# Kernel tuning notes

Hardware: AMD Instinct MI355X
Metric: run time of the kernel (lower is better)

Reference implementation:

```python
import jax, jax.numpy as jnp
import numpy as np
import math

B, D, C_LEN, Q_LEN = 32, 128, 1024, 256
NEG = -1e30

def setup_inputs() -> dict:
    key = jax.random.key(0)
    ks = jax.random.split(key, 8)
    bound = 1.0 / math.sqrt(D)
    return {
        "C": jax.random.normal(ks[0], (B, D, C_LEN), jnp.float32),
        "Q": jax.random.normal(ks[1], (B, D, Q_LEN), jnp.float32),
        "c_mask": jnp.ones((B, C_LEN), jnp.float32),
        "q_mask": jnp.ones((B, Q_LEN), jnp.float32),
        "W0": jax.random.uniform(ks[2], (3 * D,), jnp.float32, -bound, bound),
        # depthwise conv1d: in=4D groups=4D kernel=5 -> weight (4D, 1, 5)
        "dw_w": jax.random.normal(ks[3], (4 * D, 1, 5), jnp.float32) * math.sqrt(2.0 / 5),
        "dw_b": jnp.zeros((4 * D,), jnp.float32),
        # pointwise conv1d: 4D -> D, kernel 1
        "pw_w": jax.random.normal(ks[4], (D, 4 * D, 1), jnp.float32) * math.sqrt(2.0 / (4 * D)),
        "pw_b": jnp.zeros((D,), jnp.float32),
    }

def reference(C, Q, c_mask, q_mask, W0, dw_w, dw_b, pw_w, pw_b):
    d = W0.shape[0] // 3
    C_t = jnp.swapaxes(C, 1, 2)  # (B, c_len, d)
    Q_t = jnp.swapaxes(Q, 1, 2)  # (B, q_len, d)
    w1, w2, w3 = W0[:d], W0[d:2 * d], W0[2 * d:]
    # Trilinear similarity without materializing (B,c,q,3d):
    # S[b,i,j] = C_t[b,i].w1 + Q_t[b,j].w2 + sum_k C_t[b,i,k]*Q_t[b,j,k]*w3[k]
    S = (jnp.einsum('bik,bjk->bij', C_t * w3, Q_t)
         + (C_t @ w1)[:, :, None] + (Q_t @ w2)[:, None, :])  # (B, c_len, q_len)
    q_m = q_mask[:, None, :]
    c_m = c_mask[:, :, None]
    S_bar = jax.nn.softmax(S * q_m + NEG * (1.0 - q_m), axis=2)
    S_bbar = jax.nn.softmax(S * c_m + NEG * (1.0 - c_m), axis=1)
    A = jnp.einsum('bij,bjk->bik', S_bar, Q_t)                       # (B, c_len, d)
    # bmm(S_bar, S_bbar^T) @ C_t  ==  S_bar @ (S_bbar^T @ C_t)
    Bm = jnp.einsum('bij,bjk->bik', S_bar, jnp.einsum('bij,bik->bjk', S_bbar, C_t))
    out = jnp.concatenate([C_t, A, C_t * A, C_t * Bm], axis=2)       # (B, c_len, 4d)
    x = jnp.swapaxes(out, 1, 2)  # (B, 4d, c_len)
    # depthwise separable conv (eval mode: dropout is identity)
    x = jax.lax.conv_general_dilated(x, dw_w, (1,), [(2, 2)],
                                     dimension_numbers=('NCH', 'OIH', 'NCH'),
                                     feature_group_count=x.shape[1]) + dw_b[None, :, None]
    x = jax.lax.conv_general_dilated(x, pw_w, (1,), [(0, 0)],
                                     dimension_numbers=('NCH', 'OIH', 'NCH')) + pw_b[None, :, None]
    return x  # (B, d, c_len)
```

## Files before the change

### kernel.cpp

```cpp
#include <hip/hip_runtime.h>
#include <math.h>

#define NB 32
#define ND 128
#define NC 1024
#define NQ 256
#define NEGV (-1e30f)

typedef __attribute__((ext_vector_type(8))) __bf16 bf16x8;
typedef __attribute__((ext_vector_type(4))) float f32x4;
typedef __attribute__((ext_vector_type(8))) unsigned short u16x8;
typedef __attribute__((ext_vector_type(4))) unsigned short u16x4;

__device__ inline unsigned short f2bf(float f) {
  unsigned u = __builtin_bit_cast(unsigned, f);
  u += 0x7FFFu + ((u >> 16) & 1u);
  return (unsigned short)(u >> 16);
}
__device__ inline float bf2f(unsigned short u) {
  return __builtin_bit_cast(float, (unsigned)u << 16);
}

__global__ __launch_bounds__(256) void k_pwcvt(const float* __restrict__ pwW, unsigned short* __restrict__ pwB16) {
  int idx = blockIdx.x * 256 + threadIdx.x;
  const float4* src = (const float4*)pwW;
  float4 v0 = src[idx * 2], v1 = src[idx * 2 + 1];
  u16x8 o;
  o[0] = f2bf(v0.x); o[1] = f2bf(v0.y); o[2] = f2bf(v0.z); o[3] = f2bf(v0.w);
  o[4] = f2bf(v1.x); o[5] = f2bf(v1.y); o[6] = f2bf(v1.z); o[7] = f2bf(v1.w);
  ((u16x8*)pwB16)[idx] = o;
}

__global__ __launch_bounds__(256) void k_qprep(const float* __restrict__ Q, const float* __restrict__ W0,
                                               unsigned short* __restrict__ qSwz, unsigned short* __restrict__ qT,
                                               float* __restrict__ qb) {
  __shared__ unsigned short T2[128 * 66];
  __shared__ float w2L[128];
  __shared__ float qbP[4][64];
  int b = blockIdx.y, jc = blockIdx.x, j0 = jc * 64, t = threadIdx.x;
  if (t < 128) w2L[t] = W0[ND + t];
  int d = t >> 1, half = t & 1;
  const float* src = Q + ((size_t)b * ND + d) * NQ + j0 + half * 32;
  unsigned short* qdst = qSwz + ((size_t)b * ND + d) * NQ + jc * 64;
  #pragma unroll
  for (int q = 0; q < 4; ++q) {
    float4 v0 = ((const float4*)src)[q * 2];
    float4 v1 = ((const float4*)src)[q * 2 + 1];
    u16x8 o;
    o[0] = f2bf(v0.x); o[1] = f2bf(v0.y); o[2] = f2bf(v0.z); o[3] = f2bf(v0.w);
    o[4] = f2bf(v1.x); o[5] = f2bf(v1.y); o[6] = f2bf(v1.z); o[7] = f2bf(v1.w);
    *(u16x8*)&T2[d * 66 + half * 32 + q * 8] = o;
    int g = half * 4 + q;
    *(u16x8*)&qdst[(g ^ (d & 7)) * 8] = o;
  }
  __syncthreads();
  {
    int jj = t & 63, dq = t >> 6;
    float s = 0.f;
    #pragma unroll 8
    for (int k = 0; k < 32; ++k) {
      int dd = dq * 32 + k;
      s += bf2f(T2[dd * 66 + jj]) * w2L[dd];
    }
    qbP[dq][jj] = s;
  }
  __syncthreads();
  if (t < 64)
    qb[b * NQ + j0 + t] = qbP[0][t] + qbP[1][t] + qbP[2][t] + qbP[3][t];
  {
    int jj = t >> 2, p = t & 3;
    unsigned short* dst = qT + ((size_t)b * NQ + j0 + jj) * ND;
    #pragma unroll
    for (int q = 0; q < 4; ++q) {
      int g = p * 4 + q;
      u16x8 o;
      #pragma unroll
      for (int e = 0; e < 8; ++e) o[e] = T2[(g * 8 + e) * 66 + jj];
      int sg = (g & 8) | ((g & 7) ^ (jj & 7));
      *(u16x8*)&dst[sg * 8] = o;
    }
  }
}

__global__ __launch_bounds__(256) void k_cprep(const float* __restrict__ C, const float* __restrict__ W0,
                                               unsigned short* __restrict__ cw3T, unsigned short* __restrict__ cSwz,
                                               float* __restrict__ cb) {
  __shared__ unsigned short T2[128 * 66];
  __shared__ float w1L[128], w3L[128];
  __shared__ float cbP[4][64];
  int b = blockIdx.y, i0 = blockIdx.x * 64, t = threadIdx.x;
  if (t < 128) { w1L[t] = W0[t]; w3L[t] = W0[2 * ND + t]; }
  int k = t >> 1, half = t & 1;
  const float* src = C + ((size_t)b * ND + k) * NC + i0 + half * 32;
  unsigned short* cdst = cSwz + ((size_t)b * ND + k) * NC + blockIdx.x * 64;
  #pragma unroll
  for (int q = 0; q < 4; ++q) {
    float4 v0 = ((const float4*)src)[q * 2];
    float4 v1 = ((const float4*)src)[q * 2 + 1];
    u16x8 o;
    o[0] = f2bf(v0.x); o[1] = f2bf(v0.y); o[2] = f2bf(v0.z); o[3] = f2bf(v0.w);
    o[4] = f2bf(v1.x); o[5] = f2bf(v1.y); o[6] = f2bf(v1.z); o[7] = f2bf(v1.w);
    *(u16x8*)&T2[k * 66 + half * 32 + q * 8] = o;
    int g = half * 4 + q;
    *(u16x8*)&cdst[(g ^ (k & 7)) * 8] = o;
  }
  __syncthreads();
  {
    int ii = t & 63, kq = t >> 6;
    float s = 0.f;
    #pragma unroll 8
    for (int kk = 0; kk < 32; ++kk) {
      int dd = kq * 32 + kk;
      s += bf2f(T2[dd * 66 + ii]) * w1L[dd];
    }
    cbP[kq][ii] = s;
  }
  __syncthreads();
  if (t < 64)
    cb[b * NC + i0 + t] = cbP[0][t] + cbP[1][t] + cbP[2][t] + cbP[3][t];
  {
    int ii = t >> 2, p = t & 3;
    unsigned short* dst = cw3T + ((size_t)b * NC + i0 + ii) * ND;
    #pragma unroll
    for (int q = 0; q < 4; ++q) {
      int g = p * 4 + q;
      u16x8 o;
      #pragma unroll
      for (int e = 0; e < 8; ++e)
        o[e] = f2bf(bf2f(T2[(g * 8 + e) * 66 + ii]) * w3L[g * 8 + e]);
      int sg = (g & 8) | ((g & 7) ^ (ii & 7));
      *(u16x8*)&dst[sg * 8] = o;
    }
  }
}

__global__ __launch_bounds__(256) void k_stats(const unsigned short* __restrict__ cw3T,
                                               const unsigned short* __restrict__ qT,
                                               const float* __restrict__ cb, const float* __restrict__ qb,
                                               const float* __restrict__ q_mask, const float* __restrict__ c_mask,
                                               float* __restrict__ rowmax, float* __restrict__ rowsum,
                                               float* __restrict__ colPm, float* __restrict__ colPs) {
  __shared__ float rmP[64][4], rsP[64][4];
  __shared__ float cbL[64], cmL[64], qbL[256], qmL[256];
  int b = blockIdx.y, i0 = blockIdx.x * 64;
  int t = threadIdx.x, w = t >> 6, l = t & 63, h = l >> 4, lr = l & 15;
  int wj = w * 64;
  if (t < 64) { cbL[t] = cb[b * NC + i0 + t]; cmL[t] = c_mask[b * NC + i0 + t]; }
  qbL[t] = qb[b * NQ + t];
  qmL[t] = q_mask[b * NQ + t];
  const unsigned short* Arow = cw3T + ((size_t)b * NC + i0) * ND;
  const unsigned short* Brow = qT + (size_t)b * NQ * ND;
  f32x4 acc[4][4] = {};
  #pragma unroll
  for (int ks = 0; ks < 4; ++ks) {
    int g = ks * 4 + h;
    int off = ((g & 8) | ((g & 7) ^ (lr & 7))) * 8;
    bf16x8 a[4], bq[4];
    #pragma unroll
    for (int mi = 0; mi < 4; ++mi)
      a[mi] = *(const bf16x8*)&Arow[(size_t)(mi * 16 + lr) * ND + off];
    #pragma unroll
    for (int nf = 0; nf < 4; ++nf)
      bq[nf] = *(const bf16x8*)&Brow[(size_t)(wj + nf * 16 + lr) * ND + off];
    #pragma unroll
    for (int mi = 0; mi < 4; ++mi)
      #pragma unroll
      for (int nf = 0; nf < 4; ++nf)
        acc[mi][nf] = __builtin_amdgcn_mfma_f32_16x16x32_bf16(a[mi], bq[nf], acc[mi][nf], 0, 0, 0);
  }
  __syncthreads();
  float qbv[4], qmv[4];
  #pragma unroll
  for (int nf = 0; nf < 4; ++nf) {
    int j = wj + nf * 16 + lr;
    qbv[nf] = qbL[j]; qmv[nf] = qmL[j];
  }
  float rmv[4][4], rsv[4][4];
  #pragma unroll
  for (int mi = 0; mi < 4; ++mi)
    #pragma unroll
    for (int r = 0; r < 4; ++r) { rmv[mi][r] = -3.0e38f; rsv[mi][r] = 0.f; }
  #pragma unroll
  for (int mi = 0; mi < 4; ++mi) {
    #pragma unroll
    for (int r = 0; r < 4; ++r) {
      int row = mi * 16 + h * 4 + r;
      float cbr = cbL[row];
      #pragma unroll
      for (int nf = 0; nf < 4; ++nf) {
        float sv = acc[mi][nf][r] + cbr + qbv[nf];
        acc[mi][nf][r] = sv;
        float vq = sv * qmv[nf] + NEGV * (1.f - qmv[nf]);
        float mn = fmaxf(rmv[mi][r], vq);
        rsv[mi][r] = rsv[mi][r] * __expf(rmv[mi][r] - mn) + __expf(vq - mn);
        rmv[mi][r] = mn;
      }
    }
  }
  #pragma unroll
  for (int off = 1; off < 16; off <<= 1) {
    #pragma unroll
    for (int mi = 0; mi < 4; ++mi)
      #pragma unroll
      for (int r = 0; r < 4; ++r) {
        float mo = __shfl_xor(rmv[mi][r], off);
        float so = __shfl_xor(rsv[mi][r], off);
        float mn = fmaxf(rmv[mi][r], mo);
        rsv[mi][r] = rsv[mi][r] * __expf(rmv[mi][r] - mn) + so * __expf(mo - mn);
        rmv[mi][r] = mn;
      }
  }
  if (lr == 0) {
    #pragma unroll
    for (int mi = 0; mi < 4; ++mi)
      #pragma unroll
      for (int r = 0; r < 4; ++r) {
        rmP[mi * 16 + h * 4 + r][w] = rmv[mi][r];
        rsP[mi * 16 + h * 4 + r][w] = rsv[mi][r];
      }
  }
  float pm[4], ps[4];
  #pragma unroll
  for (int nf = 0; nf < 4; ++nf) { pm[nf] = -3.0e38f; ps[nf] = 0.f; }
  #pragma unroll
  for (int mi = 0; mi < 4; ++mi)
    #pragma unroll
    for (int r = 0; r < 4; ++r) {
      int row = mi * 16 + h * 4 + r;
      float cm = cmL[row];
      float cbias = NEGV * (1.f - cm);
      #pragma unroll
      for (int nf = 0; nf < 4; ++nf) {
        float v = acc[mi][nf][r] * cm + cbias;
        float mn = fmaxf(pm[nf], v);
        ps[nf] = ps[nf] * __expf(pm[nf] - mn) + __expf(v - mn);
        pm[nf] = mn;
      }
    }
  #pragma unroll
  for (int off = 16; off < 64; off <<= 1) {
    #pragma unroll
    for (int nf = 0; nf < 4; ++nf) {
      float mo = __shfl_xor(pm[nf], off);
      float so = __shfl_xor(ps[nf], off);
      float mn = fmaxf(pm[nf], mo);
      ps[nf] = ps[nf] * __expf(pm[nf] - mn) + so * __expf(mo - mn);
      pm[nf] = mn;
    }
  }
  if (h == 0) {
    #pragma unroll
    for (int nf = 0; nf < 4; ++nf) {
      int j = wj + nf * 16 + lr;
      colPm[((size_t)blockIdx.x * NB + b) * NQ + j] = pm[nf];
      colPs[((size_t)blockIdx.x * NB + b) * NQ + j] = ps[nf];
    }
  }
  __syncthreads();
  if (t < 64) {
    float m = rmP[t][0], s = rsP[t][0];
    #pragma unroll
    for (int k = 1; k < 4; ++k) {
      float mo = rmP[t][k], so = rsP[t][k];
      float mn = fmaxf(m, mo);
      s = s * __expf(m - mn) + so * __expf(mo - mn);
      m = mn;
    }
    rowmax[b * NC + i0 + t] = m;
    rowsum[b * NC + i0 + t] = s;
  }
}

__global__ __launch_bounds__(256) void k3c_combine(const float* __restrict__ colPm, const float* __restrict__ colPs,
                                                   float* __restrict__ colmax, float* __restrict__ colsum) {
  int idx = blockIdx.x * 256 + threadIdx.x;
  float m = -3.0e38f, s = 0.f;
  #pragma unroll
  for (int tl = 0; tl < 16; ++tl) {
    float mo = colPm[(size_t)tl * NB * NQ + idx];
    float so = colPs[(size_t)tl * NB * NQ + idx];
    float mn = fmaxf(m, mo);
    s = s * __expf(m - mn) + so * __expf(mo - mn);
    m = mn;
  }
  colmax[idx] = m; colsum[idx] = s;
}

__global__ __launch_bounds__(256) void k4f(const unsigned short* __restrict__ cw3T,
                                           const unsigned short* __restrict__ qT,
                                           const unsigned short* __restrict__ cSwz,
                                           const float* __restrict__ cb, const float* __restrict__ qb,
                                           const float* __restrict__ c_mask,
                                           const float* __restrict__ colmax, const float* __restrict__ colsum,
                                           float* __restrict__ partial) {
  __shared__ unsigned short Pt[32 * 72];
  __shared__ float cmxL[32], cinvL[32], qbL2[32], cbL[64], cmL[64];
  int b = blockIdx.y;
  int jt = blockIdx.x & 7, split = blockIdx.x >> 3;
  int j0 = jt * 32;
  int t = threadIdx.x, w = t >> 6, l = t & 63, h = l >> 4, lr = l & 15;
  if (t < 32) {
    cmxL[t] = colmax[b * NQ + j0 + t];
    cinvL[t] = 1.0f / colsum[b * NQ + j0 + t];
    qbL2[t] = qb[b * NQ + j0 + t];
  }
  const unsigned short* Ab = cw3T + (size_t)b * NC * ND;
  const unsigned short* Bb = qT + ((size_t)b * NQ + j0) * ND;
  const unsigned short* Cb2 = cSwz + (size_t)b * ND * NC;
  f32x4 accI[2][2] = {};
  for (int ic8 = 0; ic8 < 8; ++ic8) {
    int ic = split * 512 + ic8 * 64;
    if (t < 64) { cbL[t] = cb[b * NC + ic + t]; cmL[t] = c_mask[b * NC + ic + t]; }
    __syncthreads();
    f32x4 sA[2] = {};
    #pragma unroll
    for (int ks = 0; ks < 4; ++ks) {
      int g = ks * 4 + h;
      int off = ((g & 8) | ((g & 7) ^ (lr & 7))) * 8;
      bf16x8 av = *(const bf16x8*)&Ab[(size_t)(ic + w * 16 + lr) * ND + off];
      #pragma unroll
      for (int jf = 0; jf < 2; ++jf) {
        bf16x8 bv = *(const bf16x8*)&Bb[(size_t)(jf * 16 + lr) * ND + off];
        sA[jf] = __builtin_amdgcn_mfma_f32_16x16x32_bf16(av, bv, sA[jf], 0, 0, 0);
      }
    }
    #pragma unroll
    for (int jf = 0; jf < 2; ++jf)
      #pragma unroll
      for (int r = 0; r < 4; ++r) {
        int i_ = w * 16 + h * 4 + r;
        int j_ = jf * 16 + lr;
        float sfull = sA[jf][r] + cbL[i_] + qbL2[j_];
        float cm = cmL[i_];
        float vc = sfull * cm + NEGV * (1.f - cm);
        float p = __expf(vc - cmxL[j_]) * cinvL[j_];
        Pt[j_ * 72 + (((i_ >> 3) ^ (j_ & 7)) << 3) + (i_ & 7)] = f2bf(p);
      }
    __syncthreads();
    #pragma unroll
    for (int ks = 0; ks < 2; ++ks) {
      bf16x8 aC[2], bP[2];
      #pragma unroll
      for (int mf = 0; mf < 2; ++mf) {
        int d = w * 32 + mf * 16 + lr;
        aC[mf] = *(const bf16x8*)&Cb2[(size_t)d * NC + ic + (((ks * 4 + h) ^ (lr & 7)) * 8)];
      }
      #pragma unroll
      for (int jf = 0; jf < 2; ++jf) {
        int j_ = jf * 16 + lr;
        bP[jf] = *(const bf16x8*)&Pt[j_ * 72 + (((ks * 4 + h) ^ (j_ & 7)) * 8)];
      }
      #pragma unroll
      for (int mf = 0; mf < 2; ++mf)
        #pragma unroll
        for (int jf = 0; jf < 2; ++jf)
          accI[mf][jf] = __builtin_amdgcn_mfma_f32_16x16x32_bf16(aC[mf], bP[jf], accI[mf][jf], 0, 0, 0);
    }
  }
  float* pout = partial + ((size_t)(split * NB + b) * ND) * NQ;
  #pragma unroll
  for (int mf = 0; mf < 2; ++mf)
    #pragma unroll
    for (int jf = 0; jf < 2; ++jf)
      #pragma unroll
      for (int r = 0; r < 4; ++r) {
        int d = w * 32 + mf * 16 + h * 4 + r;
        int j = j0 + jf * 16 + lr;
        pout[(size_t)d * NQ + j] = accI[mf][jf][r];
      }
}

__global__ __launch_bounds__(256) void k4c2(const float* __restrict__ partial,
                                            unsigned short* __restrict__ iSwz) {
  int idx = blockIdx.x * 256 + threadIdx.x;
  const size_t n = (size_t)NB * ND * NQ / 4;
  const float4* p = (const float4*)partial;
  float4 a = p[idx], b4 = p[n + idx];
  u16x4 o;
  o[0] = f2bf(a.x + b4.x);
  o[1] = f2bf(a.y + b4.y);
  o[2] = f2bf(a.z + b4.z);
  o[3] = f2bf(a.w + b4.w);
  int lin = idx * 4;
  int j = lin & 255, dd = (lin >> 8) & 127, bb = lin >> 15;
  int g = (j >> 3) & 7, e0 = j & 7;
  int outoff = ((bb * 128 + dd) << 8) + (j & 192) + ((g ^ (dd & 7)) << 3) + e0;
  *(u16x4*)&iSwz[outoff] = o;
}

__global__ __launch_bounds__(256) void k5f(const unsigned short* __restrict__ cw3T,
                                           const unsigned short* __restrict__ qT,
                                           const unsigned short* __restrict__ qSwz,
                                           const unsigned short* __restrict__ iSwz,
                                           const float* __restrict__ C,
                                           const float* __restrict__ cb, const float* __restrict__ qb,
                                           const float* __restrict__ q_mask,
                                           const float* __restrict__ rowmax, const float* __restrict__ rowsum,
                                           unsigned short* __restrict__ xB) {
  extern __shared__ char sm[];
  unsigned short* cwA = (unsigned short*)sm;
  unsigned short* Pl = (unsigned short*)(sm + 8192);
  float* As = (float*)sm;
  float* Bs = (float*)(sm + 17024);
  __shared__ float rmL[32], riL[32], cbI[32], qbL[256], qmL[256];
  int b = blockIdx.y, i0 = blockIdx.x * 32;
  int t = threadIdx.x, w = t >> 6, l = t & 63, h = l >> 4, lr = l & 15;
  {
    const unsigned short* src = cw3T + ((size_t)b * NC + i0) * ND;
    #pragma unroll
    for (int k = 0; k < 2; ++k) {
      int u = t + k * 256;
      *(u16x8*)&cwA[u * 8] = *(const u16x8*)(src + u * 8);
    }
  }
  if (t < 32) {
    rmL[t] = rowmax[b * NC + i0 + t];
    riL[t] = 1.0f / rowsum[b * NC + i0 + t];
    cbI[t] = cb[b * NC + i0 + t];
  }
  qbL[t] = qb[b * NQ + t];
  qmL[t] = q_mask[b * NQ + t];
  __syncthreads();

  const unsigned short* qTb = qT + (size_t)b * NQ * ND;
  const unsigned short* qSb = qSwz + (size_t)b * ND * NQ;
  const unsigned short* iSb = iSwz + (size_t)b * ND * NQ;
  f32x4 accA[2][2] = {};
  f32x4 accB[2][2] = {};

  for (int jc = 0; jc < 4; ++jc) {
    int j0 = jc * 64;
    f32x4 sA[2] = {};
    #pragma unroll
    for (int ks = 0; ks < 4; ++ks) {
      int g = ks * 4 + h;
      int off = ((g & 8) | ((g & 7) ^ (lr & 7))) * 8;
      bf16x8 bv = *(const bf16x8*)&qTb[(size_t)(j0 + w * 16 + lr) * ND + off];
      #pragma unroll
      for (int mi = 0; mi < 2; ++mi) {
        bf16x8 av = *(const bf16x8*)&cwA[(mi * 16 + lr) * 128 + off];
        sA[mi] = __builtin_amdgcn_mfma_f32_16x16x32_bf16(av, bv, sA[mi], 0, 0, 0);
      }
    }
    #pragma unroll
    for (int mi = 0; mi < 2; ++mi)
      #pragma unroll
      for (int r = 0; r < 4; ++r) {
        int i_ = mi * 16 + h * 4 + r;
        int j_ = w * 16 + lr;
        float sfull = sA[mi][r] + cbI[i_] + qbL[j0 + j_];
        float qm = qmL[j0 + j_];
        float vq = sfull * qm + NEGV * (1.f - qm);
        float p = __expf(vq - rmL[i_]) * riL[i_];
        Pl[i_ * 72 + (((j_ >> 3) ^ (i_ & 7)) << 3) + (j_ & 7)] = f2bf(p);
      }
    __syncthreads();
    #pragma unroll
    for (int ks = 0; ks < 2; ++ks) {
      bf16x8 aP[2], bQ[2], bI[2];
      #pragma unroll
      for (int mi = 0; mi < 2; ++mi) {
        int i = mi * 16 + lr;
        int slot = (ks * 4 + h) ^ (i & 7);
        aP[mi] = *(const bf16x8*)&Pl[i * 72 + slot * 8];
      }
      #pragma unroll
      for (int nd = 0; nd < 2; ++nd) {
        int d = w * 32 + nd * 16 + lr;
        int slot = (ks * 4 + h) ^ (d & 7);
        bQ[nd] = *(const bf16x8*)&qSb[(size_t)d * NQ + j0 + slot * 8];
        bI[nd] = *(const bf16x8*)&iSb[(size_t)d * NQ + j0 + slot * 8];
      }
      #pragma unroll
      for (int mi = 0; mi < 2; ++mi)
        #pragma unroll
        for (int nd = 0; nd < 2; ++nd) {
          accA[mi][nd] = __builtin_amdgcn_mfma_f32_16x16x32_bf16(aP[mi], bQ[nd], accA[mi][nd], 0, 0, 0);
          accB[mi][nd] = __builtin_amdgcn_mfma_f32_16x16x32_bf16(aP[mi], bI[nd], accB[mi][nd], 0, 0, 0);
        }
    }
    __syncthreads();
  }
  #pragma unroll
  for (int mi = 0; mi < 2; ++mi)
    #pragma unroll
    for (int nd = 0; nd < 2; ++nd) {
      int d = w * 32 + nd * 16 + lr;
      #pragma unroll
      for (int r = 0; r < 4; ++r) {
        int i = mi * 16 + h * 4 + r;
        As[i * 133 + d] = accA[mi][nd][r];
        Bs[i * 133 + d] = accB[mi][nd][r];
      }
    }
  __syncthreads();
  {
    int i4 = (t & 7) * 4, db = t >> 3;
    const float* Cb = C + (size_t)b * ND * NC;
    unsigned short* xb = xB + (size_t)b * 4 * ND * NC;
    #pragma unroll
    for (int p = 0; p < 4; ++p) {
      int d = db + p * 32;
      float4 c4 = *(const float4*)&Cb[(size_t)d * NC + i0 + i4];
      float4 a4, b4;
      a4.x = As[(i4 + 0) * 133 + d]; a4.y = As[(i4 + 1) * 133 + d];
      a4.z = As[(i4 + 2) * 133 + d]; a4.w = As[(i4 + 3) * 133 + d];
      b4.x = Bs[(i4 + 0) * 133 + d]; b4.y = Bs[(i4 + 1) * 133 + d];
      b4.z = Bs[(i4 + 2) * 133 + d]; b4.w = Bs[(i4 + 3) * 133 + d];
      u16x4 o0, o1, o2, o3;
      o0[0] = f2bf(c4.x); o0[1] = f2bf(c4.y); o0[2] = f2bf(c4.z); o0[3] = f2bf(c4.w);
      o1[0] = f2bf(a4.x); o1[1] = f2bf(a4.y); o1[2] = f2bf(a4.z); o1[3] = f2bf(a4.w);
      o2[0] = f2bf(c4.x * a4.x); o2[1] = f2bf(c4.y * a4.y); o2[2] = f2bf(c4.z * a4.z); o2[3] = f2bf(c4.w * a4.w);
      o3[0] = f2bf(c4.x * b4.x); o3[1] = f2bf(c4.y * b4.y); o3[2] = f2bf(c4.z * b4.z); o3[3] = f2bf(c4.w * b4.w);
      *(u16x4*)&xb[(size_t)(0 * ND + d) * NC + i0 + i4] = o0;
      *(u16x4*)&xb[(size_t)(1 * ND + d) * NC + i0 + i4] = o1;
      *(u16x4*)&xb[(size_t)(2 * ND + d) * NC + i0 + i4] = o2;
      *(u16x4*)&xb[(size_t)(3 * ND + d) * NC + i0 + i4] = o3;
    }
  }
}

__global__ __launch_bounds__(256) void k6_mfma(const unsigned short* __restrict__ x,
                                               const float* __restrict__ dwW, const float* __restrict__ dwB,
                                               const unsigned short* __restrict__ pwB16,
                                               const float* __restrict__ pwB, float* __restrict__ out) {
  extern __shared__ char sm6[];
  unsigned short* xs = (unsigned short*)sm6;
  unsigned short* x1s = (unsigned short*)(sm6 + 7168);
  unsigned short* pws = (unsigned short*)(sm6 + 11776);
  int b = blockIdx.y, l0 = blockIdx.x * 32;
  int t = threadIdx.x, w = t >> 6, l = t & 63, h = l >> 4, lr = l & 15;
  const unsigned short* xb = x + (size_t)b * 4 * ND * NC;
  f32x4 acc[2][2] = {};
  int cgw = t & 63, lb = w * 8;

  for (int ch = 0; ch < 8; ++ch) {
    int cg0 = ch * 64;
    __syncthreads();
    #pragma unroll
    for (int k = 0; k < 2; ++k) {
      int id2 = t + k * 256;
      if (id2 < 384) {
        int row = id2 / 6, seg = id2 % 6;
        int gl = l0 - 8 + seg * 8;
        u16x8 v = {};
        if ((unsigned)gl <= 1016u)
          v = *(const u16x8*)(xb + (size_t)(cg0 + row) * NC + gl);
        *(u16x8*)&xs[row * 56 + seg * 8] = v;
      }
    }
    #pragma unroll
    for (int k = 0; k < 4; ++k) {
      int id2 = t + k * 256;
      int o = id2 >> 3, s8 = id2 & 7;
      *(u16x8*)&pws[o * 72 + s8 * 8] = *(const u16x8*)(pwB16 + (size_t)o * 512 + cg0 + s8 * 8);
    }
    __syncthreads();
    {
      int gch = cg0 + cgw;
      float bias = dwB[gch];
      float dwv[5];
      #pragma unroll
      for (int tp = 0; tp < 5; ++tp) dwv[tp] = dwW[gch * 5 + tp];
      float f[24];
      #pragma unroll
      for (int s = 0; s < 3; ++s) {
        u16x8 v = *(const u16x8*)&xs[cgw * 56 + lb + s * 8];
        #pragma unroll
        for (int e = 0; e < 8; ++e) f[s * 8 + e] = bf2f(v[e]);
      }
      #pragma unroll
      for (int e = 0; e < 8; ++e) {
        float a = bias;
        #pragma unroll
        for (int tp = 0; tp < 5; ++tp)
          a = fmaf(f[e + 6 + tp], dwv[tp], a);
        x1s[(lb + e) * 72 + cgw] = f2bf(a);
      }
    }
    __syncthreads();
    #pragma unroll
    for (int ks = 0; ks < 2; ++ks) {
      bf16x8 aW[2], bX[2];
      #pragma unroll
      for (int mi = 0; mi < 2; ++mi) {
        int o = w * 32 + mi * 16 + lr;
        aW[mi] = *(const bf16x8*)&pws[o * 72 + ks * 32 + h * 8];
      }
      #pragma unroll
      for (int nf = 0; nf < 2; ++nf) {
        int ll = nf * 16 + lr;
        bX[nf] = *(const bf16x8*)&x1s[ll * 72 + ks * 32 + h * 8];
      }
      #pragma unroll
      for (int mi = 0; mi < 2; ++mi)
        #pragma unroll
        for (int nf = 0; nf < 2; ++nf)
          acc[mi][nf] = __builtin_amdgcn_mfma_f32_16x16x32_bf16(aW[mi], bX[nf], acc[mi][nf], 0, 0, 0);
    }
  }
  #pragma unroll
  for (int mi = 0; mi < 2; ++mi) {
    #pragma unroll
    for (int r = 0; r < 4; ++r) {
      int o = w * 32 + mi * 16 + h * 4 + r;
      float bv = pwB[o];
      #pragma unroll
      for (int nf = 0; nf < 2; ++nf)
        out[((size_t)b * ND + o) * NC + l0 + nf * 16 + lr] = acc[mi][nf][r] + bv;
    }
  }
}

extern "C" void kernel_launch(void* const* d_in, const int* in_sizes, int n_in,
                              void* d_out, int out_size, void* d_ws, size_t ws_size,
                              hipStream_t stream) {
  const float* C = (const float*)d_in[0];
  const float* Q = (const float*)d_in[1];
  const float* c_mask = (const float*)d_in[2];
  const float* q_mask = (const float*)d_in[3];
  const float* W0 = (const float*)d_in[4];
  const float* dwW = (const float*)d_in[5];
  const float* dwB = (const float*)d_in[6];
  const float* pwW = (const float*)d_in[7];
  const float* pwB = (const float*)d_in[8];
  float* out = (float*)d_out;
  float* ws = (float*)d_ws;

  float* rowmax = ws;
  float* rowsum = rowmax + NB * NC;
  float* colmax = rowsum + NB * NC;
  float* colsum = colmax + NB * NQ;
  float* cb = colsum + NB * NQ;
  float* qb = cb + NB * NC;
  float* colPm = qb + NB * NQ;
  float* colPs = colPm + 16 * NB * NQ;
  unsigned short* qSwz = (unsigned short*)(colPs + 16 * NB * NQ);
  unsigned short* qT = qSwz + (size_t)NB * ND * NQ;
  unsigned short* iSwz = qT + (size_t)NB * NQ * ND;
  unsigned short* cw3T = iSwz + (size_t)NB * ND * NQ;
  unsigned short* cSwz = cw3T + (size_t)NB * NC * ND;
  unsigned short* pwB16 = cSwz + (size_t)NB * ND * NC;
  float* partial = (float*)(pwB16 + ND * 512);
  unsigned short* xB = (unsigned short*)(partial + 2 * (size_t)NB * ND * NQ);

  k_pwcvt<<<dim3(32), 256, 0, stream>>>(pwW, pwB16);
  k_qprep<<<dim3(4, NB), 256, 0, stream>>>(Q, W0, qSwz, qT, qb);
  k_cprep<<<dim3(16, NB), 256, 0, stream>>>(C, W0, cw3T, cSwz, cb);
  k_stats<<<dim3(16, NB), 256, 0, stream>>>(cw3T, qT, cb, qb, q_mask, c_mask, rowmax, rowsum, colPm, colPs);
  k3c_combine<<<dim3(NB * NQ / 256), 256, 0, stream>>>(colPm, colPs, colmax, colsum);
  k4f<<<dim3(16, NB), 256, 0, stream>>>(cw3T, qT, cSwz, cb, qb, c_mask, colmax, colsum, partial);
  k4c2<<<dim3(NB * ND * NQ / 4 / 256), 256, 0, stream>>>(partial, iSwz);
  k5f<<<dim3(NC / 32, NB), 256, 34048, stream>>>(cw3T, qT, qSwz, iSwz, C, cb, qb, q_mask, rowmax, rowsum, xB);
  k6_mfma<<<dim3(NC / 32, NB), 256, 30208, stream>>>(xB, dwW, dwB, pwB16, pwB, out);
}
```

Before: 119.4 us.

## Read bf16 C in k5f and retile depthwise/pointwise conv kernel to 64-wide

k5f now reads the already-converted swizzled bf16 copy of C instead of the fp32 original, halving that read and reusing the bf16 values directly for the first output slice. The conv kernel is restructured into k6f: each block covers 64 positions instead of 32, the depthwise stage reads x straight from global memory rather than staging it in shared memory, and the pointwise weights are loaded straight from global memory into MFMA fragments. Each wave now computes a 64x32 output tile with more accumulators. This is meant to cut global traffic, shared-memory staging and sync overhead, at the cost of more register pressure and uncoalesced, uncached-in-LDS weight loads.

```diff
diff --git a/kernel.cpp b/kernel.cpp
--- a/kernel.cpp
+++ b/kernel.cpp
@@ -392,7 +392,7 @@
                                            const unsigned short* __restrict__ qT,
                                            const unsigned short* __restrict__ qSwz,
                                            const unsigned short* __restrict__ iSwz,
-                                           const float* __restrict__ C,
+                                           const unsigned short* __restrict__ cSwz,
                                            const float* __restrict__ cb, const float* __restrict__ qb,
                                            const float* __restrict__ q_mask,
                                            const float* __restrict__ rowmax, const float* __restrict__ rowsum,
@@ -496,23 +496,26 @@
   __syncthreads();
   {
     int i4 = (t & 7) * 4, db = t >> 3;
-    const float* Cb = C + (size_t)b * ND * NC;
+    const unsigned short* cSb = cSwz + (size_t)b * ND * NC;
     unsigned short* xb = xB + (size_t)b * 4 * ND * NC;
+    int ib = i0 + i4;
     #pragma unroll
     for (int p = 0; p < 4; ++p) {
       int d = db + p * 32;
-      float4 c4 = *(const float4*)&Cb[(size_t)d * NC + i0 + i4];
+      u16x4 c4b = *(const u16x4*)&cSb[(size_t)d * NC + (ib & ~63) + ((((ib >> 3) & 7) ^ (d & 7)) << 3) + (i4 & 7)];
+      float cx[4];
+      #pragma unroll
+      for (int e = 0; e < 4; ++e) cx[e] = bf2f(c4b[e]);
       float4 a4, b4;
       a4.x = As[(i4 + 0) * 133 + d]; a4.y = As[(i4 + 1) * 133 + d];
       a4.z = As[(i4 + 2) * 133 + d]; a4.w = As[(i4 + 3) * 133 + d];
       b4.x = Bs[(i4 + 0) * 133 + d]; b4.y = Bs[(i4 + 1) * 133 + d];
       b4.z = Bs[(i4 + 2) * 133 + d]; b4.w = Bs[(i4 + 3) * 133 + d];
-      u16x4 o0, o1, o2, o3;
-      o0[0] = f2bf(c4.x); o0[1] = f2bf(c4.y); o0[2] = f2bf(c4.z); o0[3] = f2bf(c4.w);
+      u16x4 o1, o2, o3;
       o1[0] = f2bf(a4.x); o1[1] = f2bf(a4.y); o1[2] = f2bf(a4.z); o1[3] = f2bf(a4.w);
-      o2[0] = f2bf(c4.x * a4.x); o2[1] = f2bf(c4.y * a4.y); o2[2] = f2bf(c4.z * a4.z); o2[3] = f2bf(c4.w * a4.w);
-      o3[0] = f2bf(c4.x * b4.x); o3[1] = f2bf(c4.y * b4.y); o3[2] = f2bf(c4.z * b4.z); o3[3] = f2bf(c4.w * b4.w);
-      *(u16x4*)&xb[(size_t)(0 * ND + d) * NC + i0 + i4] = o0;
+      o2[0] = f2bf(cx[0] * a4.x); o2[1] = f2bf(cx[1] * a4.y); o2[2] = f2bf(cx[2] * a4.z); o2[3] = f2bf(cx[3] * a4.w);
+      o3[0] = f2bf(cx[0] * b4.x); o3[1] = f2bf(cx[1] * b4.y); o3[2] = f2bf(cx[2] * b4.z); o3[3] = f2bf(cx[3] * b4.w);
+      *(u16x4*)&xb[(size_t)(0 * ND + d) * NC + i0 + i4] = c4b;
       *(u16x4*)&xb[(size_t)(1 * ND + d) * NC + i0 + i4] = o1;
       *(u16x4*)&xb[(size_t)(2 * ND + d) * NC + i0 + i4] = o2;
       *(u16x4*)&xb[(size_t)(3 * ND + d) * NC + i0 + i4] = o3;
@@ -520,94 +523,73 @@
   }
 }
 
-__global__ __launch_bounds__(256) void k6_mfma(const unsigned short* __restrict__ x,
-                                               const float* __restrict__ dwW, const float* __restrict__ dwB,
-                                               const unsigned short* __restrict__ pwB16,
-                                               const float* __restrict__ pwB, float* __restrict__ out) {
-  extern __shared__ char sm6[];
-  unsigned short* xs = (unsigned short*)sm6;
-  unsigned short* x1s = (unsigned short*)(sm6 + 7168);
-  unsigned short* pws = (unsigned short*)(sm6 + 11776);
-  int b = blockIdx.y, l0 = blockIdx.x * 32;
+__global__ __launch_bounds__(256) void k6f(const unsigned short* __restrict__ xB,
+                                           const float* __restrict__ dwW, const float* __restrict__ dwB,
+                                           const unsigned short* __restrict__ pwB16,
+                                           const float* __restrict__ pwB, float* __restrict__ out) {
+  __shared__ unsigned short x1s[64 * 72];
+  int b = blockIdx.y, l0 = blockIdx.x * 64;
   int t = threadIdx.x, w = t >> 6, l = t & 63, h = l >> 4, lr = l & 15;
-  const unsigned short* xb = x + (size_t)b * 4 * ND * NC;
-  f32x4 acc[2][2] = {};
-  int cgw = t & 63, lb = w * 8;
+  int wo = (w >> 1) * 64, wl = (w & 1) * 32;
+  int cg = t & 63, lq = t >> 6;
+  const unsigned short* xb = xB + (size_t)b * 4 * ND * NC;
+  f32x4 acc[4][2] = {};
 
   for (int ch = 0; ch < 8; ++ch) {
     int cg0 = ch * 64;
     __syncthreads();
-    #pragma unroll
-    for (int k = 0; k < 2; ++k) {
-      int id2 = t + k * 256;
-      if (id2 < 384) {
-        int row = id2 / 6, seg = id2 % 6;
-        int gl = l0 - 8 + seg * 8;
-        u16x8 v = {};
-        if ((unsigned)gl <= 1016u)
-          v = *(const u16x8*)(xb + (size_t)(cg0 + row) * NC + gl);
-        *(u16x8*)&xs[row * 56 + seg * 8] = v;
-      }
-    }
-    #pragma unroll
-    for (int k = 0; k < 4; ++k) {
-      int id2 = t + k * 256;
-      int o = id2 >> 3, s8 = id2 & 7;
-      *(u16x8*)&pws[o * 72 + s8 * 8] = *(const u16x8*)(pwB16 + (size_t)o * 512 + cg0 + s8 * 8);
-    }
-    __syncthreads();
     {
-      int gch = cg0 + cgw;
+      int gch = cg0 + cg;
       float bias = dwB[gch];
       float dwv[5];
       #pragma unroll
       for (int tp = 0; tp < 5; ++tp) dwv[tp] = dwW[gch * 5 + tp];
-      float f[24];
-      #pragma unroll
-      for (int s = 0; s < 3; ++s) {
-        u16x8 v = *(const u16x8*)&xs[cgw * 56 + lb + s * 8];
+      float f[32];
+      const unsigned short* xrow = xb + (size_t)gch * NC;
+      #pragma unroll
+      for (int s = 0; s < 4; ++s) {
+        int gl = l0 + lq * 16 - 8 + s * 8;
+        u16x8 v = {};
+        if ((unsigned)gl <= 1016u) v = *(const u16x8*)(xrow + gl);
         #pragma unroll
         for (int e = 0; e < 8; ++e) f[s * 8 + e] = bf2f(v[e]);
       }
       #pragma unroll
-      for (int e = 0; e < 8; ++e) {
+      for (int e = 0; e < 16; ++e) {
         float a = bias;
         #pragma unroll
         for (int tp = 0; tp < 5; ++tp)
           a = fmaf(f[e + 6 + tp], dwv[tp], a);
-        x1s[(lb + e) * 72 + cgw] = f2bf(a);
+        x1s[(lq * 16 + e) * 72 + cg] = f2bf(a);
       }
     }
     __syncthreads();
     #pragma unroll
     for (int ks = 0; ks < 2; ++ks) {
-      bf16x8 aW[2], bX[2];
-      #pragma unroll
-      for (int mi = 0; mi < 2; ++mi) {
-        int o = w * 32 + mi * 16 + lr;
-        aW[mi] = *(const bf16x8*)&pws[o * 72 + ks * 32 + h * 8];
-      }
-      #pragma unroll
-      for (int nf = 0; nf < 2; ++nf) {
-        int ll = nf * 16 + lr;
-        bX[nf] = *(const bf16x8*)&x1s[ll * 72 + ks * 32 + h * 8];
-      }
-      #pragma unroll
-      for (int mi = 0; mi < 2; ++mi)
+      int koff = cg0 + (ks * 4 + h) * 8;
+      bf16x8 aW[4], bX[2];
+      #pragma unroll
+      for (int mf = 0; mf < 4; ++mf)
+        aW[mf] = *(const bf16x8*)&pwB16[(size_t)(wo + mf * 16 + lr) * 512 + koff];
+      #pragma unroll
+      for (int nf = 0; nf < 2; ++nf)
+        bX[nf] = *(const bf16x8*)&x1s[(wl + nf * 16 + lr) * 72 + (ks * 4 + h) * 8];
+      #pragma unroll
+      for (int mf = 0; mf < 4; ++mf)
         #pragma unroll
         for (int nf = 0; nf < 2; ++nf)
-          acc[mi][nf] = __builtin_amdgcn_mfma_f32_16x16x32_bf16(aW[mi], bX[nf], acc[mi][nf], 0, 0, 0);
-    }
-  }
-  #pragma unroll
-  for (int mi = 0; mi < 2; ++mi) {
+          acc[mf][nf] = __builtin_amdgcn_mfma_f32_16x16x32_bf16(aW[mf], bX[nf], acc[mf][nf], 0, 0, 0);
+    }
+  }
+  #pragma unroll
+  for (int mf = 0; mf < 4; ++mf) {
     #pragma unroll
     for (int r = 0; r < 4; ++r) {
-      int o = w * 32 + mi * 16 + h * 4 + r;
+      int o = wo + mf * 16 + h * 4 + r;
       float bv = pwB[o];
       #pragma unroll
       for (int nf = 0; nf < 2; ++nf)
-        out[((size_t)b * ND + o) * NC + l0 + nf * 16 + lr] = acc[mi][nf][r] + bv;
+        out[((size_t)b * ND + o) * NC + l0 + wl + nf * 16 + lr] = acc[mf][nf][r] + bv;
     }
   }
 }
@@ -651,6 +633,6 @@
   k3c_combine<<<dim3(NB * NQ / 256), 256, 0, stream>>>(colPm, colPs, colmax, colsum);
   k4f<<<dim3(16, NB), 256, 0, stream>>>(cw3T, qT, cSwz, cb, qb, c_mask, colmax, colsum, partial);
   k4c2<<<dim3(NB * ND * NQ / 4 / 256), 256, 0, stream>>>(partial, iSwz);
-  k5f<<<dim3(NC / 32, NB), 256, 34048, stream>>>(cw3T, qT, qSwz, iSwz, C, cb, qb, q_mask, rowmax, rowsum, xB);
-  k6_mfma<<<dim3(NC / 32, NB), 256, 30208, stream>>>(xB, dwW, dwB, pwB16, pwB, out);
-}
+  k5f<<<dim3(NC / 32, NB), 256, 34048, stream>>>(cw3T, qT, qSwz, iSwz, cSwz, cb, qb, q_mask, rowmax, rowsum, xB);
+  k6f<<<dim3(NC / 64, NB), 256, 0, stream>>>(xB, dwW, dwB, pwB16, pwB, out);
+}
```

New measurement: 123.9 us. 1.04x slower.
